# Optimization experiments

Hardware: AMD Instinct MI355X
Metric: run time of the kernel (lower is better)

The kernel has to match this reference:

```python
import jax, jax.numpy as jnp
import numpy as np

B, T, I, H = 256, 500, 128, 512
CLIP = 5.0

def setup_inputs() -> dict:
    key = jax.random.key(0)
    ks = jax.random.split(key, 6)
    x = jax.random.normal(ks[0], (B, T, I), dtype=jnp.float32)
    h_0 = jax.random.normal(ks[1], (B, H), dtype=jnp.float32)
    # variance-scaled init per init_variance_scaling_ with scale_dim = I + H (is_encoder=True)
    scale = I + H
    w_ih = jax.random.normal(ks[2], (3 * H, I), dtype=jnp.float32) / np.sqrt(scale)
    w_hh = jax.random.normal(ks[3], (3 * H, H), dtype=jnp.float32) / np.sqrt(scale)
    b_ih = jnp.concatenate([jnp.ones(2 * H, jnp.float32), jnp.zeros(H, jnp.float32)])
    b_hh = jnp.zeros(3 * H, jnp.float32)
    return {"x": x, "h_0": h_0, "w_ih": w_ih, "w_hh": w_hh, "b_ih": b_ih, "b_hh": b_hh}

def _gru_scan(x, h_0, w_ih, w_hh, b_ih, b_hh, clip_value):
    # Precompute input projections for all timesteps in one big GEMM: [B,T,3H]
    xi = jnp.einsum('bti,gi->btg', x, w_ih) + b_ih
    xi_t = jnp.transpose(xi, (1, 0, 2))  # [T,B,3H]
    Hs = h_0.shape[-1]

    def step(h, xg):
        hg = h @ w_hh.T + b_hh  # [B,3H]
        x_r, x_z, x_n = xg[:, :Hs], xg[:, Hs:2*Hs], xg[:, 2*Hs:]
        h_r, h_z, h_n = hg[:, :Hs], hg[:, Hs:2*Hs], hg[:, 2*Hs:]
        r = jax.nn.sigmoid(x_r + h_r)
        z = jax.nn.sigmoid(x_z + h_z)
        n = jnp.tanh(x_n + r * h_n)
        h_new = (1.0 - z) * n + z * h
        h_new = jnp.clip(h_new, -clip_value, clip_value)
        return h_new, h_new

    h_last, out = jax.lax.scan(step, h_0, xi_t)
    return jnp.transpose(out, (1, 0, 2)), h_last  # [B,T,H], [B,H]

def reference(x, h_0, w_ih, w_hh, b_ih, b_hh):
    return _gru_scan(x, h_0, w_ih, w_hh, b_ih, b_hh, CLIP)
```

## Files before the change

### kernel.cpp

```cpp
#include <hip/hip_runtime.h>
#include <hip/hip_bf16.h>


#define T_STEPS 500
#define B_TOT   256
#define I_DIM   128
#define H_DIM   512
#define BB      16
#define UU      32
#define TPAD    512
#define FLAGS_BYTES (16 * TPAD * 16)

typedef __bf16 bf16x8 __attribute__((ext_vector_type(8)));
typedef float  f32x4  __attribute__((ext_vector_type(4)));
typedef float  f32x8  __attribute__((ext_vector_type(8)));

__device__ __forceinline__ bf16x8 cvt8(const float* p) {
    f32x8 v = *(const f32x8*)p;
    bf16x8 r;
#pragma unroll
    for (int i = 0; i < 8; ++i) r[i] = (__bf16)v[i];
    return r;
}

__device__ __forceinline__ float fast_sigmoid(float x) {
    float e = __builtin_amdgcn_exp2f(-1.4426950408889634f * x);
    return __builtin_amdgcn_rcpf(1.0f + e);
}
__device__ __forceinline__ float fast_tanh(float x) {
    float e = __builtin_amdgcn_exp2f(2.8853900817779268f * x);
    return 1.0f - 2.0f * __builtin_amdgcn_rcpf(1.0f + e);
}

__global__ __launch_bounds__(512, 2)
void gru_persist(const float* __restrict__ x,
                 const float* __restrict__ h0,
                 const float* __restrict__ wih,
                 const float* __restrict__ whh,
                 const float* __restrict__ bih,
                 const float* __restrict__ bhh,
                 float* __restrict__ out,
                 unsigned char* __restrict__ flags,
                 __hip_bfloat16* __restrict__ hbuf)
{
    const int tid  = threadIdx.x;
    const int bx   = blockIdx.x;
    const int g    = bx >> 4;
    const int j    = bx & 15;
    const int bg   = g * BB;
    const int u0   = j * UU;
    const int w    = tid >> 6;
    const int lane = tid & 63;
    const int lrow = lane & 15;
    const int lq   = lane >> 4;

    __shared__ float s_g[4][16 * 36];
    __shared__ float s_hold[16 * 32];
    __shared__ float s_bih[96];
    __shared__ float s_bhh[96];
    __shared__ __hip_bfloat16 s_h[16 * 512];

    {
        int b = tid >> 5, u = tid & 31;
        s_hold[b * 32 + u] = h0[(size_t)(bg + b) * H_DIM + u0 + u];
        if (tid < 96) {
            int gg = tid >> 5, uu = tid & 31;
            s_bih[tid] = bih[gg * H_DIM + u0 + uu];
            s_bhh[tid] = bhh[gg * H_DIM + u0 + uu];
        }
    }

    const int gate = w >> 1;
    const int hf   = w & 1;
    bf16x8 wf[16], wfi[4];
    if (w < 6) {
        const long row0 = (long)gate * H_DIM + u0 + 16 * hf;
        const float* wr  = whh + (row0 + lrow) * H_DIM + lq * 8;
        const float* wr2 = wih + (row0 + lrow) * I_DIM + lq * 8;
#pragma unroll
        for (int kt = 0; kt < 16; ++kt) wf[kt] = cvt8(wr + kt * 32);
#pragma unroll
        for (int kt = 0; kt < 4; ++kt)  wfi[kt] = cvt8(wr2 + kt * 32);
    }
    __syncthreads();

    const int sr = tid >> 5, sc = tid & 31;
    char* sd0 = (char*)s_h + sr * 1024 + ((sc * 32     ) ^ ((sr & 7) << 4));
    char* sd1 = (char*)s_h + sr * 1024 + ((sc * 32 + 16) ^ ((sr & 7) << 4));

    int sync_ok = 1;

#pragma unroll 1
    for (int t = 0; t < T_STEPS; ++t) {
        f32x4 accA = {0, 0, 0, 0}, accB = {0, 0, 0, 0}, accX = {0, 0, 0, 0};

        bf16x8 xf0, xf1, xf2, xf3;
        if (w < 6) {
            const float* xr =
                x + ((size_t)(bg + lrow) * T_STEPS + t) * I_DIM + lq * 8;
            xf0 = cvt8(xr);
            xf1 = cvt8(xr + 32);
            xf2 = cvt8(xr + 64);
            xf3 = cvt8(xr + 96);
        }

        if (t > 0 && sync_ok) {
            const unsigned long long* fl = (const unsigned long long*)
                (flags + ((size_t)g * TPAD + (t - 1)) * 16);
            long tries = 0;
            for (;;) {
                unsigned long long a = __hip_atomic_load(
                    fl, __ATOMIC_RELAXED, __HIP_MEMORY_SCOPE_AGENT);
                unsigned long long b = __hip_atomic_load(
                    fl + 1, __ATOMIC_RELAXED, __HIP_MEMORY_SCOPE_AGENT);
                if (a == 0x0101010101010101ull &&
                    b == 0x0101010101010101ull) break;
                __builtin_amdgcn_s_sleep(1);
                if (++tries > (1L << 20)) { sync_ok = 0; break; }
            }
        }
        asm volatile("" ::: "memory");

        bf16x8 sv0, sv1;
        if (t == 0) {
            const float* hp = h0 + (size_t)(bg + sr) * H_DIM + sc * 16;
            sv0 = cvt8(hp);
            sv1 = cvt8(hp + 8);
        } else {
            const unsigned long long* hp = (const unsigned long long*)
                (hbuf + (size_t)(t & 1) * B_TOT * H_DIM +
                 (size_t)(bg + sr) * H_DIM + sc * 16);
            unsigned long long q0 = __hip_atomic_load(
                hp + 0, __ATOMIC_RELAXED, __HIP_MEMORY_SCOPE_AGENT);
            unsigned long long q1 = __hip_atomic_load(
                hp + 1, __ATOMIC_RELAXED, __HIP_MEMORY_SCOPE_AGENT);
            unsigned long long q2 = __hip_atomic_load(
                hp + 2, __ATOMIC_RELAXED, __HIP_MEMORY_SCOPE_AGENT);
            unsigned long long q3 = __hip_atomic_load(
                hp + 3, __ATOMIC_RELAXED, __HIP_MEMORY_SCOPE_AGENT);
            union { unsigned long long q[2]; bf16x8 v; } ua, ub;
            ua.q[0] = q0; ua.q[1] = q1;
            ub.q[0] = q2; ub.q[1] = q3;
            sv0 = ua.v;
            sv1 = ub.v;
        }

        if (w < 6) {
            f32x4 ai = {0, 0, 0, 0};
            ai = __builtin_amdgcn_mfma_f32_16x16x32_bf16(xf0, wfi[0], ai, 0, 0, 0);
            ai = __builtin_amdgcn_mfma_f32_16x16x32_bf16(xf1, wfi[1], ai, 0, 0, 0);
            ai = __builtin_amdgcn_mfma_f32_16x16x32_bf16(xf2, wfi[2], ai, 0, 0, 0);
            ai = __builtin_amdgcn_mfma_f32_16x16x32_bf16(xf3, wfi[3], ai, 0, 0, 0);
            if (gate < 2) accA = ai; else accX = ai;
        }

        *(bf16x8*)sd0 = sv0;
        *(bf16x8*)sd1 = sv1;
        __syncthreads();

        if (w < 6) {
            const char* ab  = (const char*)s_h + lrow * 1024;
            const int   swz = (lrow & 7) << 4;
#pragma unroll
            for (int kt = 0; kt < 8; ++kt) {
                bf16x8 hfr = *(const bf16x8*)(ab + ((lq * 16 + kt * 64) ^ swz));
                accA = __builtin_amdgcn_mfma_f32_16x16x32_bf16(hfr, wf[kt],
                                                               accA, 0, 0, 0);
            }
#pragma unroll
            for (int kt = 8; kt < 16; ++kt) {
                bf16x8 hfr = *(const bf16x8*)(ab + ((lq * 16 + kt * 64) ^ swz));
                accB = __builtin_amdgcn_mfma_f32_16x16x32_bf16(hfr, wf[kt],
                                                               accB, 0, 0, 0);
            }
            const int col = hf * 16 + lrow;
#pragma unroll
            for (int i = 0; i < 4; ++i) {
                int b = lq * 4 + i;
                s_g[gate][b * 36 + col] = accA[i] + accB[i];
                if (gate == 2) s_g[3][b * 36 + col] = accX[i];
            }
        }
        __syncthreads();

        if (tid < 128) {
            const int b  = tid >> 3;
            const int ub = (tid & 7) * 4;
            f32x4 vr  = *(const f32x4*)&s_g[0][b * 36 + ub];
            f32x4 vz  = *(const f32x4*)&s_g[1][b * 36 + ub];
            f32x4 vhn = *(const f32x4*)&s_g[2][b * 36 + ub];
            f32x4 vxn = *(const f32x4*)&s_g[3][b * 36 + ub];
            f32x4 hold = *(const f32x4*)&s_hold[b * 32 + ub];
            f32x4 hnew;
            unsigned long long pk = 0;
#pragma unroll
            for (int i = 0; i < 4; ++i) {
                float rr = fast_sigmoid(vr[i] + s_bih[ub + i] + s_bhh[ub + i]);
                float zz = fast_sigmoid(vz[i] + s_bih[32 + ub + i] +
                                        s_bhh[32 + ub + i]);
                float nn = fast_tanh(vxn[i] + s_bih[64 + ub + i] +
                                     rr * (vhn[i] + s_bhh[64 + ub + i]));
                float hv = (1.0f - zz) * nn + zz * hold[i];
                hv = fminf(fmaxf(hv, -5.0f), 5.0f);
                hnew[i] = hv;
                __bf16 hb = (__bf16)hv;
                pk |= (unsigned long long)__builtin_bit_cast(unsigned short, hb)
                      << (16 * i);
            }
            *(f32x4*)&s_hold[b * 32 + ub] = hnew;
            *(f32x4*)(out + ((size_t)(bg + b) * T_STEPS + t) * H_DIM + u0 + ub)
                = hnew;
            __hip_atomic_store(
                (unsigned long long*)(hbuf +
                    (size_t)((t + 1) & 1) * B_TOT * H_DIM +
                    (size_t)(bg + b) * H_DIM + u0 + ub),
                pk, __ATOMIC_RELAXED, __HIP_MEMORY_SCOPE_AGENT);
            if (t == T_STEPS - 1)
                *(f32x4*)(out + (size_t)B_TOT * T_STEPS * H_DIM +
                          (size_t)(bg + b) * H_DIM + u0 + ub) = hnew;
        }
        __syncthreads();

        if (tid == 0 && t < T_STEPS - 1) {
            __hip_atomic_store(flags + ((size_t)g * TPAD + t) * 16 + j,
                               (unsigned char)1, __ATOMIC_RELAXED,
                               __HIP_MEMORY_SCOPE_AGENT);
        }
    }
}

extern "C" void kernel_launch(void* const* d_in, const int* in_sizes, int n_in,
                              void* d_out, int out_size, void* d_ws, size_t ws_size,
                              hipStream_t stream) {
    const float* x   = (const float*)d_in[0];
    const float* h0  = (const float*)d_in[1];
    const float* wih = (const float*)d_in[2];
    const float* whh = (const float*)d_in[3];
    const float* bih = (const float*)d_in[4];
    const float* bhh = (const float*)d_in[5];
    float* out = (float*)d_out;
    unsigned char*  flags = (unsigned char*)d_ws;
    __hip_bfloat16* hbuf  = (__hip_bfloat16*)((char*)d_ws + FLAGS_BYTES);

    hipMemsetAsync(d_ws, 0, FLAGS_BYTES, stream);

    void* args[] = { (void*)&x, (void*)&h0, (void*)&wih, (void*)&whh,
                     (void*)&bih, (void*)&bhh, (void*)&out,
                     (void*)&flags, (void*)&hbuf };
    hipLaunchCooperativeKernel((void*)gru_persist, dim3(256), dim3(512),
                               args, 0, stream);
}
```

Before: 2.027 ms.

## Replace per-step flag barrier with step-tagged hidden-state words for inter-block sync

```diff
diff --git a/kernel.cpp b/kernel.cpp
--- a/kernel.cpp
+++ b/kernel.cpp
@@ -8,12 +8,13 @@
 #define H_DIM   512
 #define BB      16
 #define UU      32
-#define TPAD    512
-#define FLAGS_BYTES (16 * TPAD * 16)
 
 typedef __bf16 bf16x8 __attribute__((ext_vector_type(8)));
 typedef float  f32x4  __attribute__((ext_vector_type(4)));
 typedef float  f32x8  __attribute__((ext_vector_type(8)));
+typedef unsigned short u16;
+typedef unsigned int   u32;
+typedef unsigned long long u64;
 
 __device__ __forceinline__ bf16x8 cvt8(const float* p) {
     f32x8 v = *(const f32x8*)p;
@@ -31,6 +32,20 @@
     float e = __builtin_amdgcn_exp2f(2.8853900817779268f * x);
     return 1.0f - 2.0f * __builtin_amdgcn_rcpf(1.0f + e);
 }
+
+#define BAR_LDS()                                              \
+    do {                                                       \
+        asm volatile("s_waitcnt lgkmcnt(0)" ::: "memory");     \
+        __builtin_amdgcn_sched_barrier(0);                     \
+        __builtin_amdgcn_s_barrier();                          \
+        __builtin_amdgcn_sched_barrier(0);                     \
+    } while (0)
+#define BAR_RAW()                                              \
+    do {                                                       \
+        __builtin_amdgcn_sched_barrier(0);                     \
+        __builtin_amdgcn_s_barrier();                          \
+        __builtin_amdgcn_sched_barrier(0);                     \
+    } while (0)
 
 __global__ __launch_bounds__(512, 2)
 void gru_persist(const float* __restrict__ x,
@@ -40,8 +55,7 @@
                  const float* __restrict__ bih,
                  const float* __restrict__ bhh,
                  float* __restrict__ out,
-                 unsigned char* __restrict__ flags,
-                 __hip_bfloat16* __restrict__ hbuf)
+                 u32* __restrict__ hbuf)
 {
     const int tid  = threadIdx.x;
     const int bx   = blockIdx.x;
@@ -87,6 +101,8 @@
     const int sr = tid >> 5, sc = tid & 31;
     char* sd0 = (char*)s_h + sr * 1024 + ((sc * 32     ) ^ ((sr & 7) << 4));
     char* sd1 = (char*)s_h + sr * 1024 + ((sc * 32 + 16) ^ ((sr & 7) << 4));
+    const u64* hp0 = (const u64*)(hbuf + (size_t)(bg + sr) * H_DIM + sc * 16);
+    const u64* hp1 = (const u64*)((const u32*)hp0 + (size_t)B_TOT * H_DIM);
 
     int sync_ok = 1;
 
@@ -104,45 +120,13 @@
             xf3 = cvt8(xr + 96);
         }
 
-        if (t > 0 && sync_ok) {
-            const unsigned long long* fl = (const unsigned long long*)
-                (flags + ((size_t)g * TPAD + (t - 1)) * 16);
-            long tries = 0;
-            for (;;) {
-                unsigned long long a = __hip_atomic_load(
-                    fl, __ATOMIC_RELAXED, __HIP_MEMORY_SCOPE_AGENT);
-                unsigned long long b = __hip_atomic_load(
-                    fl + 1, __ATOMIC_RELAXED, __HIP_MEMORY_SCOPE_AGENT);
-                if (a == 0x0101010101010101ull &&
-                    b == 0x0101010101010101ull) break;
-                __builtin_amdgcn_s_sleep(1);
-                if (++tries > (1L << 20)) { sync_ok = 0; break; }
-            }
-        }
-        asm volatile("" ::: "memory");
-
-        bf16x8 sv0, sv1;
-        if (t == 0) {
-            const float* hp = h0 + (size_t)(bg + sr) * H_DIM + sc * 16;
-            sv0 = cvt8(hp);
-            sv1 = cvt8(hp + 8);
-        } else {
-            const unsigned long long* hp = (const unsigned long long*)
-                (hbuf + (size_t)(t & 1) * B_TOT * H_DIM +
-                 (size_t)(bg + sr) * H_DIM + sc * 16);
-            unsigned long long q0 = __hip_atomic_load(
-                hp + 0, __ATOMIC_RELAXED, __HIP_MEMORY_SCOPE_AGENT);
-            unsigned long long q1 = __hip_atomic_load(
-                hp + 1, __ATOMIC_RELAXED, __HIP_MEMORY_SCOPE_AGENT);
-            unsigned long long q2 = __hip_atomic_load(
-                hp + 2, __ATOMIC_RELAXED, __HIP_MEMORY_SCOPE_AGENT);
-            unsigned long long q3 = __hip_atomic_load(
-                hp + 3, __ATOMIC_RELAXED, __HIP_MEMORY_SCOPE_AGENT);
-            union { unsigned long long q[2]; bf16x8 v; } ua, ub;
-            ua.q[0] = q0; ua.q[1] = q1;
-            ub.q[0] = q2; ub.q[1] = q3;
-            sv0 = ua.v;
-            sv1 = ub.v;
+        const u64* hp = (t & 1) ? hp1 : hp0;
+        u64 q[8];
+        if (t > 0) {
+#pragma unroll
+            for (int i = 0; i < 8; ++i)
+                q[i] = __hip_atomic_load(hp + i, __ATOMIC_RELAXED,
+                                         __HIP_MEMORY_SCOPE_AGENT);
         }
 
         if (w < 6) {
@@ -154,9 +138,42 @@
             if (gate < 2) accA = ai; else accX = ai;
         }
 
+        bf16x8 sv0, sv1;
+        if (t == 0) {
+            const float* hps = h0 + (size_t)(bg + sr) * H_DIM + sc * 16;
+            sv0 = cvt8(hps);
+            sv1 = cvt8(hps + 8);
+        } else {
+            const u64 expect = ((u64)(u32)t << 16) | ((u64)(u32)t << 48);
+            const u64 mask   = 0xFFFF0000FFFF0000ull;
+            long tries = 0;
+            while (sync_ok) {
+                u64 m = 0;
+#pragma unroll
+                for (int i = 0; i < 8; ++i) m |= (q[i] & mask) ^ expect;
+                if (m == 0) break;
+                __builtin_amdgcn_s_sleep(1);
+                if (++tries > (1L << 20)) { sync_ok = 0; break; }
+#pragma unroll
+                for (int i = 0; i < 8; ++i)
+                    q[i] = __hip_atomic_load(hp + i, __ATOMIC_RELAXED,
+                                             __HIP_MEMORY_SCOPE_AGENT);
+            }
+            union { u16 s[8]; bf16x8 v; } ua, ub;
+#pragma unroll
+            for (int i = 0; i < 4; ++i) {
+                ua.s[2 * i]     = (u16)q[i];
+                ua.s[2 * i + 1] = (u16)(q[i] >> 32);
+                ub.s[2 * i]     = (u16)q[4 + i];
+                ub.s[2 * i + 1] = (u16)(q[4 + i] >> 32);
+            }
+            sv0 = ua.v;
+            sv1 = ub.v;
+        }
+
         *(bf16x8*)sd0 = sv0;
         *(bf16x8*)sd1 = sv1;
-        __syncthreads();
+        BAR_LDS();
 
         if (w < 6) {
             const char* ab  = (const char*)s_h + lrow * 1024;
@@ -181,7 +198,7 @@
                 if (gate == 2) s_g[3][b * 36 + col] = accX[i];
             }
         }
-        __syncthreads();
+        BAR_LDS();
 
         if (tid < 128) {
             const int b  = tid >> 3;
@@ -192,7 +209,8 @@
             f32x4 vxn = *(const f32x4*)&s_g[3][b * 36 + ub];
             f32x4 hold = *(const f32x4*)&s_hold[b * 32 + ub];
             f32x4 hnew;
-            unsigned long long pk = 0;
+            u32 wd[4];
+            const u32 tagw = (u32)(t + 1) << 16;
 #pragma unroll
             for (int i = 0; i < 4; ++i) {
                 float rr = fast_sigmoid(vr[i] + s_bih[ub + i] + s_bhh[ub + i]);
@@ -204,28 +222,24 @@
                 hv = fminf(fmaxf(hv, -5.0f), 5.0f);
                 hnew[i] = hv;
                 __bf16 hb = (__bf16)hv;
-                pk |= (unsigned long long)__builtin_bit_cast(unsigned short, hb)
-                      << (16 * i);
+                wd[i] = tagw | (u32)__builtin_bit_cast(u16, hb);
+            }
+            if (t < T_STEPS - 1) {
+                u64* dst = (u64*)(hbuf + (size_t)((t + 1) & 1) * B_TOT * H_DIM +
+                                  (size_t)(bg + b) * H_DIM + u0 + ub);
+                __hip_atomic_store(dst, (u64)wd[0] | ((u64)wd[1] << 32),
+                                   __ATOMIC_RELAXED, __HIP_MEMORY_SCOPE_AGENT);
+                __hip_atomic_store(dst + 1, (u64)wd[2] | ((u64)wd[3] << 32),
+                                   __ATOMIC_RELAXED, __HIP_MEMORY_SCOPE_AGENT);
             }
             *(f32x4*)&s_hold[b * 32 + ub] = hnew;
             *(f32x4*)(out + ((size_t)(bg + b) * T_STEPS + t) * H_DIM + u0 + ub)
                 = hnew;
-            __hip_atomic_store(
-                (unsigned long long*)(hbuf +
-                    (size_t)((t + 1) & 1) * B_TOT * H_DIM +
-                    (size_t)(bg + b) * H_DIM + u0 + ub),
-                pk, __ATOMIC_RELAXED, __HIP_MEMORY_SCOPE_AGENT);
             if (t == T_STEPS - 1)
                 *(f32x4*)(out + (size_t)B_TOT * T_STEPS * H_DIM +
                           (size_t)(bg + b) * H_DIM + u0 + ub) = hnew;
         }
-        __syncthreads();
-
-        if (tid == 0 && t < T_STEPS - 1) {
-            __hip_atomic_store(flags + ((size_t)g * TPAD + t) * 16 + j,
-                               (unsigned char)1, __ATOMIC_RELAXED,
-                               __HIP_MEMORY_SCOPE_AGENT);
-        }
+        BAR_RAW();
     }
 }
 
@@ -239,14 +253,11 @@
     const float* bih = (const float*)d_in[4];
     const float* bhh = (const float*)d_in[5];
     float* out = (float*)d_out;
-    unsigned char*  flags = (unsigned char*)d_ws;
-    __hip_bfloat16* hbuf  = (__hip_bfloat16*)((char*)d_ws + FLAGS_BYTES);
-
-    hipMemsetAsync(d_ws, 0, FLAGS_BYTES, stream);
+    u32* hbuf = (u32*)d_ws;
+
 
     void* args[] = { (void*)&x, (void*)&h0, (void*)&wih, (void*)&whh,
-                     (void*)&bih, (void*)&bhh, (void*)&out,
-                     (void*)&flags, (void*)&hbuf };
+                     (void*)&bih, (void*)&bhh, (void*)&out, (void*)&hbuf };
     hipLaunchCooperativeKernel((void*)gru_persist, dim3(256), dim3(512),
                                args, 0, stream);
 }
```

Result: slower. 2.598 ms (+28.1%).
